# Optimization experiments

Measured on AMD Instinct MI355X. Metric: run time of the kernel, lower is better.

Reference implementation:

```python
import jax, jax.numpy as jnp
import numpy as np

# Constants from __init__ (domain bounds)
X_MIN, X_MAX = -1.0, 1.0
Y_MIN, Y_MAX = -1.0, 1.0
T_MIN, T_MAX = 0.0, 1.0

N_POINTS = 262144
WIDTH = 128
N_HIDDEN_STACK = 5  # hidden->hidden layers between first and last


def setup_inputs() -> dict:
    key = jax.random.key(0)
    ks = jax.random.split(key, 8)
    X = jax.random.uniform(ks[0], (N_POINTS, 4), dtype=jnp.float32)
    # glorot_normal-ish init
    def glorot(k, fan_in, fan_out, shape):
        std = (2.0 / (fan_in + fan_out)) ** 0.5
        return jax.random.normal(k, shape, dtype=jnp.float32) * std
    W0 = glorot(ks[1], 4, WIDTH, (4, WIDTH))
    b0 = jnp.zeros((WIDTH,), dtype=jnp.float32)
    Wh = glorot(ks[2], WIDTH, WIDTH, (N_HIDDEN_STACK, WIDTH, WIDTH))
    bh = jnp.zeros((N_HIDDEN_STACK, WIDTH), dtype=jnp.float32)
    WL = glorot(ks[3], WIDTH, 2, (WIDTH, 2))
    bL = jnp.zeros((2,), dtype=jnp.float32)
    nu_min = jnp.zeros((), dtype=jnp.float32)
    nu_max = jnp.ones((), dtype=jnp.float32)
    return {"X": X, "nu_min": nu_min, "nu_max": nu_max,
            "W0": W0, "b0": b0, "Wh": Wh, "bh": bh, "WL": WL, "bL": bL}


def _swish(x):
    return x * jax.nn.sigmoid(x)


def reference(X, nu_min, nu_max, W0, b0, Wh, bh, WL, bL):
    # Input rescaling to [-1, 1] per feature, then concat
    x_s = 2.0 * (X[:, 0:1] - X_MIN) / (X_MAX - X_MIN) - 1.0
    y_s = 2.0 * (X[:, 1:2] - Y_MIN) / (Y_MAX - Y_MIN) - 1.0
    t_s = 2.0 * (X[:, 2:3] - T_MIN) / (T_MAX - T_MIN) - 1.0
    nu_s = 2.0 * (X[:, 3:4] - nu_min) / (nu_max - nu_min) - 1.0
    H = jnp.concatenate([x_s, y_s, t_s, nu_s], axis=1)  # [N, 4]
    # Stacked small dense + swish layers (fused-MLP candidate)
    H = _swish(H @ W0 + b0)  # [N, WIDTH]
    for i in range(Wh.shape[0]):
        H = _swish(H @ Wh[i] + bh[i])
    return H @ WL + bL  # [N, 2], no activation on output layer
```

## Files before the change

### kernel.cpp

```cpp
#include <hip/hip_runtime.h>

typedef __bf16 bf16x8 __attribute__((ext_vector_type(8)));
typedef float  f32x4  __attribute__((ext_vector_type(4)));

#define WS_WT0_B 0
#define WS_WTH_B 8192
#define WS_WLT_B 172032

__device__ __forceinline__ unsigned short f2b(float f) {
  return __builtin_bit_cast(unsigned short, (__bf16)f);
}

__global__ void prep_kernel(const float* __restrict__ W0,
                            const float* __restrict__ Wh,
                            const float* __restrict__ WL,
                            unsigned short* __restrict__ ws) {
  int i = blockIdx.x * 256 + threadIdx.x;
  int l  = (i >> 3) & 63;
  int j  = i & 7;
  int lm = l & 15, lh = l >> 4;
  if (i < 4096) {
    int nt = i >> 9;
    int n = nt * 16 + lm, k = lh * 8 + j;
    ws[i] = f2b(k < 4 ? W0[k * 128 + n] : 0.f);
  } else if (i < 86016) {
    int t = i - 4096;
    int frag = t >> 9;
    int nt = frag & 7, ks = (frag >> 3) & 3, h = frag >> 5;
    int n = nt * 16 + lm, k = ks * 32 + lh * 8 + j;
    ws[i] = f2b(Wh[(h * 128 + k) * 128 + n]);
  } else if (i < 88064) {
    int t = i - 86016;
    int ks = t >> 9;
    int n = lm, k = ks * 32 + lh * 8 + j;
    ws[i] = f2b(n < 2 ? WL[k * 2 + n] : 0.f);
  }
}

__device__ __forceinline__ f32x4 swish4(f32x4 z) {
  f32x4 e;
  e[0] = __expf(-z[0]); e[1] = __expf(-z[1]);
  e[2] = __expf(-z[2]); e[3] = __expf(-z[3]);
  const f32x4 w = e + 1.f;
  f32x4 s;
  s[0] = __builtin_amdgcn_rcpf(w[0]); s[1] = __builtin_amdgcn_rcpf(w[1]);
  s[2] = __builtin_amdgcn_rcpf(w[2]); s[3] = __builtin_amdgcn_rcpf(w[3]);
  return z * s;
}

__launch_bounds__(64, 4)
__global__ void mlp_kernel(const float* __restrict__ X,
                           const float* __restrict__ nu_min_p,
                           const float* __restrict__ nu_max_p,
                           const float* __restrict__ b0,
                           const float* __restrict__ bh,
                           const float* __restrict__ bL,
                           const unsigned short* __restrict__ ws,
                           float* __restrict__ out) {
  __shared__ __align__(16) char Hs[32 * 256];
  const int lane = threadIdx.x;
  const int lm = lane & 15, lh = lane >> 4;
  const int row0 = blockIdx.x * 32;
  const char* wsb = reinterpret_cast<const char*>(ws);
  const int xorm = (lm & 7) << 4;

  if (lane < 32) {
    const float4 xv = reinterpret_cast<const float4*>(X)[row0 + lane];
    const float numin = nu_min_p[0], numax = nu_max_p[0];
    const float v0 = xv.x;
    const float v1 = xv.y;
    const float v2 = 2.f * xv.z - 1.f;
    const float v3 = 2.f * (xv.w - numin) / (numax - numin) - 1.f;
    uint4 c0;
    c0.x = (unsigned)f2b(v0) | ((unsigned)f2b(v1) << 16);
    c0.y = (unsigned)f2b(v2) | ((unsigned)f2b(v3) << 16);
    c0.z = 0u; c0.w = 0u;
    const uint4 z4 = make_uint4(0u, 0u, 0u, 0u);
    const int xr = (lane & 7) << 4;
    char* rp = Hs + lane * 256;
    *reinterpret_cast<uint4*>(rp + (0  ^ xr)) = c0;
    *reinterpret_cast<uint4*>(rp + (16 ^ xr)) = z4;
    *reinterpret_cast<uint4*>(rp + (32 ^ xr)) = z4;
    *reinterpret_cast<uint4*>(rp + (48 ^ xr)) = z4;
  }

  f32x4 acc[8][2];

  {
#pragma unroll
    for (int nt = 0; nt < 8; ++nt) {
      const f32x4 bv = *reinterpret_cast<const f32x4*>(b0 + nt * 16 + lh * 4);
      acc[nt][0] = bv; acc[nt][1] = bv;
    }
    bf16x8 bfr[2];
#pragma unroll
    for (int pt = 0; pt < 2; ++pt) {
      const int p = pt * 16 + lm;
      bfr[pt] = __builtin_bit_cast(bf16x8,
          *reinterpret_cast<const uint4*>(Hs + p * 256 + ((lh * 16) ^ xorm)));
    }
#pragma unroll
    for (int nt = 0; nt < 8; ++nt) {
      const bf16x8 a = __builtin_bit_cast(bf16x8,
          *reinterpret_cast<const uint4*>(wsb + WS_WT0_B + nt * 1024 + lane * 16));
      acc[nt][0] = __builtin_amdgcn_mfma_f32_16x16x32_bf16(a, bfr[0], acc[nt][0], 0, 0, 0);
      acc[nt][1] = __builtin_amdgcn_mfma_f32_16x16x32_bf16(a, bfr[1], acc[nt][1], 0, 0, 0);
    }
#pragma unroll
    for (int nt = 0; nt < 8; ++nt) {
#pragma unroll
      for (int pt = 0; pt < 2; ++pt) {
        const f32x4 r4 = swish4(acc[nt][pt]);
        unsigned short q0 = f2b(r4[0]), q1 = f2b(r4[1]), q2 = f2b(r4[2]), q3 = f2b(r4[3]);
        uint2 wv;
        wv.x = (unsigned)q0 | ((unsigned)q1 << 16);
        wv.y = (unsigned)q2 | ((unsigned)q3 << 16);
        const int p = pt * 16 + lm;
        *reinterpret_cast<uint2*>(Hs + p * 256 + (((nt * 16 + lh * 4) * 2) ^ xorm)) = wv;
      }
    }
  }

#pragma unroll 1
  for (int h = 0; h < 5; ++h) {
    const char* wbase = wsb + WS_WTH_B + h * 32768;
    const float* bias = bh + h * 128;
#pragma unroll
    for (int nt = 0; nt < 8; ++nt) {
      const f32x4 bv = *reinterpret_cast<const f32x4*>(bias + nt * 16 + lh * 4);
      acc[nt][0] = bv; acc[nt][1] = bv;
    }
#pragma unroll 1
    for (int ks = 0; ks < 4; ++ks) {
      bf16x8 bfr[2];
#pragma unroll
      for (int pt = 0; pt < 2; ++pt) {
        const int p = pt * 16 + lm;
        bfr[pt] = __builtin_bit_cast(bf16x8,
            *reinterpret_cast<const uint4*>(Hs + p * 256 + ((ks * 64 + lh * 16) ^ xorm)));
      }
#pragma unroll
      for (int nt = 0; nt < 8; ++nt) {
        const bf16x8 a = __builtin_bit_cast(bf16x8,
            *reinterpret_cast<const uint4*>(wbase + (ks * 8 + nt) * 1024 + lane * 16));
        acc[nt][0] = __builtin_amdgcn_mfma_f32_16x16x32_bf16(a, bfr[0], acc[nt][0], 0, 0, 0);
        acc[nt][1] = __builtin_amdgcn_mfma_f32_16x16x32_bf16(a, bfr[1], acc[nt][1], 0, 0, 0);
      }
    }
#pragma unroll
    for (int nt = 0; nt < 8; ++nt) {
#pragma unroll
      for (int pt = 0; pt < 2; ++pt) {
        const f32x4 r4 = swish4(acc[nt][pt]);
        unsigned short q0 = f2b(r4[0]), q1 = f2b(r4[1]), q2 = f2b(r4[2]), q3 = f2b(r4[3]);
        uint2 wv;
        wv.x = (unsigned)q0 | ((unsigned)q1 << 16);
        wv.y = (unsigned)q2 | ((unsigned)q3 << 16);
        const int p = pt * 16 + lm;
        *reinterpret_cast<uint2*>(Hs + p * 256 + (((nt * 16 + lh * 4) * 2) ^ xorm)) = wv;
      }
    }
  }

  {
    const float bl0 = bL[0], bl1 = bL[1];
#pragma unroll
    for (int pt2 = 0; pt2 < 2; ++pt2) {
      f32x4 accL = {0.f, 0.f, 0.f, 0.f};
      const int p = pt2 * 16 + lm;
#pragma unroll
      for (int ks = 0; ks < 4; ++ks) {
        const bf16x8 bfr = __builtin_bit_cast(bf16x8,
            *reinterpret_cast<const uint4*>(Hs + p * 256 + ((ks * 64 + lh * 16) ^ xorm)));
        const bf16x8 a = __builtin_bit_cast(bf16x8,
            *reinterpret_cast<const uint4*>(wsb + WS_WLT_B + ks * 1024 + lane * 16));
        accL = __builtin_amdgcn_mfma_f32_16x16x32_bf16(a, bfr, accL, 0, 0, 0);
      }
      if (lh == 0) {
        float2 o;
        o.x = accL[0] + bl0;
        o.y = accL[1] + bl1;
        *reinterpret_cast<float2*>(out + (size_t)(row0 + p) * 2) = o;
      }
    }
  }
}

extern "C" void kernel_launch(void* const* d_in, const int* in_sizes, int n_in,
                              void* d_out, int out_size, void* d_ws, size_t ws_size,
                              hipStream_t stream) {
  const float* X     = (const float*)d_in[0];
  const float* numin = (const float*)d_in[1];
  const float* numax = (const float*)d_in[2];
  const float* W0    = (const float*)d_in[3];
  const float* b0    = (const float*)d_in[4];
  const float* Wh    = (const float*)d_in[5];
  const float* bh    = (const float*)d_in[6];
  const float* WL    = (const float*)d_in[7];
  const float* bL    = (const float*)d_in[8];
  unsigned short* ws = (unsigned short*)d_ws;
  float* out = (float*)d_out;

  hipLaunchKernelGGL(prep_kernel, dim3(344), dim3(256), 0, stream, W0, Wh, WL, ws);
  hipLaunchKernelGGL(mlp_kernel, dim3(8192), dim3(64), 0, stream,
                     X, numin, numax, b0, bh, bL, ws, out);
}
```

Before: 81.65 us.

## Pack four waves per block, fully unroll layers, fold bias into MFMA init

```diff
diff --git a/kernel.cpp b/kernel.cpp
--- a/kernel.cpp
+++ b/kernel.cpp
@@ -1,6 +1,7 @@
 #include <hip/hip_runtime.h>
 
 typedef __bf16 bf16x8 __attribute__((ext_vector_type(8)));
+typedef __bf16 bf16x2 __attribute__((ext_vector_type(2)));
 typedef float  f32x4  __attribute__((ext_vector_type(4)));
 
 #define WS_WT0_B 0
@@ -48,7 +49,16 @@
   return z * s;
 }
 
-__launch_bounds__(64, 4)
+__device__ __forceinline__ uint2 pack4(f32x4 r) {
+  bf16x2 lo = {(__bf16)r[0], (__bf16)r[1]};
+  bf16x2 hi = {(__bf16)r[2], (__bf16)r[3]};
+  uint2 wv;
+  wv.x = __builtin_bit_cast(unsigned int, lo);
+  wv.y = __builtin_bit_cast(unsigned int, hi);
+  return wv;
+}
+
+__launch_bounds__(256, 4)
 __global__ void mlp_kernel(const float* __restrict__ X,
                            const float* __restrict__ nu_min_p,
                            const float* __restrict__ nu_max_p,
@@ -57,12 +67,20 @@
                            const float* __restrict__ bL,
                            const unsigned short* __restrict__ ws,
                            float* __restrict__ out) {
-  __shared__ __align__(16) char Hs[32 * 256];
-  const int lane = threadIdx.x;
+  __shared__ __align__(16) char HsAll[4][32 * 256];
+  const int lane = threadIdx.x & 63;
+  const int wave = threadIdx.x >> 6;
+  char* Hs = HsAll[wave];
   const int lm = lane & 15, lh = lane >> 4;
-  const int row0 = blockIdx.x * 32;
+  const int row0 = blockIdx.x * 128 + wave * 32;
   const char* wsb = reinterpret_cast<const char*>(ws);
+  const char* ap  = wsb + lane * 16;
   const int xorm = (lm & 7) << 4;
+
+  const int va0 = lm * 256 + ((lh * 16) ^ xorm);
+  const int va1 = va0 + 16 * 256;
+  const int wa0 = lm * 256 + ((lh * 8) ^ xorm);
+  const int wa1 = wa0 + 16 * 256;
 
   if (lane < 32) {
     const float4 xv = reinterpret_cast<const float4*>(X)[row0 + lane];
@@ -87,77 +105,59 @@
   f32x4 acc[8][2];
 
   {
+    bf16x8 bfr[2];
+    bfr[0] = __builtin_bit_cast(bf16x8, *reinterpret_cast<const uint4*>(Hs + va0));
+    bfr[1] = __builtin_bit_cast(bf16x8, *reinterpret_cast<const uint4*>(Hs + va1));
 #pragma unroll
     for (int nt = 0; nt < 8; ++nt) {
       const f32x4 bv = *reinterpret_cast<const f32x4*>(b0 + nt * 16 + lh * 4);
-      acc[nt][0] = bv; acc[nt][1] = bv;
-    }
-    bf16x8 bfr[2];
-#pragma unroll
-    for (int pt = 0; pt < 2; ++pt) {
-      const int p = pt * 16 + lm;
-      bfr[pt] = __builtin_bit_cast(bf16x8,
-          *reinterpret_cast<const uint4*>(Hs + p * 256 + ((lh * 16) ^ xorm)));
+      const bf16x8 a = __builtin_bit_cast(bf16x8,
+          *reinterpret_cast<const uint4*>(ap + WS_WT0_B + nt * 1024));
+      acc[nt][0] = __builtin_amdgcn_mfma_f32_16x16x32_bf16(a, bfr[0], bv, 0, 0, 0);
+      acc[nt][1] = __builtin_amdgcn_mfma_f32_16x16x32_bf16(a, bfr[1], bv, 0, 0, 0);
     }
 #pragma unroll
     for (int nt = 0; nt < 8; ++nt) {
-      const bf16x8 a = __builtin_bit_cast(bf16x8,
-          *reinterpret_cast<const uint4*>(wsb + WS_WT0_B + nt * 1024 + lane * 16));
-      acc[nt][0] = __builtin_amdgcn_mfma_f32_16x16x32_bf16(a, bfr[0], acc[nt][0], 0, 0, 0);
-      acc[nt][1] = __builtin_amdgcn_mfma_f32_16x16x32_bf16(a, bfr[1], acc[nt][1], 0, 0, 0);
-    }
-#pragma unroll
-    for (int nt = 0; nt < 8; ++nt) {
 #pragma unroll
       for (int pt = 0; pt < 2; ++pt) {
-        const f32x4 r4 = swish4(acc[nt][pt]);
-        unsigned short q0 = f2b(r4[0]), q1 = f2b(r4[1]), q2 = f2b(r4[2]), q3 = f2b(r4[3]);
-        uint2 wv;
-        wv.x = (unsigned)q0 | ((unsigned)q1 << 16);
-        wv.y = (unsigned)q2 | ((unsigned)q3 << 16);
-        const int p = pt * 16 + lm;
-        *reinterpret_cast<uint2*>(Hs + p * 256 + (((nt * 16 + lh * 4) * 2) ^ xorm)) = wv;
-      }
-    }
-  }
-
-#pragma unroll 1
+        const uint2 wv = pack4(swish4(acc[nt][pt]));
+        const int wa = (pt ? wa1 : wa0) ^ (nt << 5);
+        *reinterpret_cast<uint2*>(Hs + wa) = wv;
+      }
+    }
+  }
+
+#pragma unroll
   for (int h = 0; h < 5; ++h) {
-    const char* wbase = wsb + WS_WTH_B + h * 32768;
     const float* bias = bh + h * 128;
 #pragma unroll
-    for (int nt = 0; nt < 8; ++nt) {
-      const f32x4 bv = *reinterpret_cast<const f32x4*>(bias + nt * 16 + lh * 4);
-      acc[nt][0] = bv; acc[nt][1] = bv;
-    }
-#pragma unroll 1
     for (int ks = 0; ks < 4; ++ks) {
       bf16x8 bfr[2];
-#pragma unroll
-      for (int pt = 0; pt < 2; ++pt) {
-        const int p = pt * 16 + lm;
-        bfr[pt] = __builtin_bit_cast(bf16x8,
-            *reinterpret_cast<const uint4*>(Hs + p * 256 + ((ks * 64 + lh * 16) ^ xorm)));
-      }
+      bfr[0] = __builtin_bit_cast(bf16x8,
+          *reinterpret_cast<const uint4*>(Hs + (va0 ^ (ks << 6))));
+      bfr[1] = __builtin_bit_cast(bf16x8,
+          *reinterpret_cast<const uint4*>(Hs + (va1 ^ (ks << 6))));
 #pragma unroll
       for (int nt = 0; nt < 8; ++nt) {
         const bf16x8 a = __builtin_bit_cast(bf16x8,
-            *reinterpret_cast<const uint4*>(wbase + (ks * 8 + nt) * 1024 + lane * 16));
-        acc[nt][0] = __builtin_amdgcn_mfma_f32_16x16x32_bf16(a, bfr[0], acc[nt][0], 0, 0, 0);
-        acc[nt][1] = __builtin_amdgcn_mfma_f32_16x16x32_bf16(a, bfr[1], acc[nt][1], 0, 0, 0);
+            *reinterpret_cast<const uint4*>(ap + WS_WTH_B + h * 32768 + (ks * 8 + nt) * 1024));
+        if (ks == 0) {
+          const f32x4 bv = *reinterpret_cast<const f32x4*>(bias + nt * 16 + lh * 4);
+          acc[nt][0] = __builtin_amdgcn_mfma_f32_16x16x32_bf16(a, bfr[0], bv, 0, 0, 0);
+          acc[nt][1] = __builtin_amdgcn_mfma_f32_16x16x32_bf16(a, bfr[1], bv, 0, 0, 0);
+        } else {
+          acc[nt][0] = __builtin_amdgcn_mfma_f32_16x16x32_bf16(a, bfr[0], acc[nt][0], 0, 0, 0);
+          acc[nt][1] = __builtin_amdgcn_mfma_f32_16x16x32_bf16(a, bfr[1], acc[nt][1], 0, 0, 0);
+        }
       }
     }
 #pragma unroll
     for (int nt = 0; nt < 8; ++nt) {
 #pragma unroll
       for (int pt = 0; pt < 2; ++pt) {
-        const f32x4 r4 = swish4(acc[nt][pt]);
-        unsigned short q0 = f2b(r4[0]), q1 = f2b(r4[1]), q2 = f2b(r4[2]), q3 = f2b(r4[3]);
-        uint2 wv;
-        wv.x = (unsigned)q0 | ((unsigned)q1 << 16);
-        wv.y = (unsigned)q2 | ((unsigned)q3 << 16);
-        const int p = pt * 16 + lm;
-        *reinterpret_cast<uint2*>(Hs + p * 256 + (((nt * 16 + lh * 4) * 2) ^ xorm)) = wv;
+        const uint2 wv = pack4(swish4(acc[nt][pt]));
+        const int wa = (pt ? wa1 : wa0) ^ (nt << 5);
+        *reinterpret_cast<uint2*>(Hs + wa) = wv;
       }
     }
   }
@@ -165,18 +165,18 @@
   {
     const float bl0 = bL[0], bl1 = bL[1];
 #pragma unroll
-    for (int pt2 = 0; pt2 < 2; ++pt2) {
+    for (int pt = 0; pt < 2; ++pt) {
       f32x4 accL = {0.f, 0.f, 0.f, 0.f};
-      const int p = pt2 * 16 + lm;
 #pragma unroll
       for (int ks = 0; ks < 4; ++ks) {
         const bf16x8 bfr = __builtin_bit_cast(bf16x8,
-            *reinterpret_cast<const uint4*>(Hs + p * 256 + ((ks * 64 + lh * 16) ^ xorm)));
+            *reinterpret_cast<const uint4*>(Hs + ((pt ? va1 : va0) ^ (ks << 6))));
         const bf16x8 a = __builtin_bit_cast(bf16x8,
-            *reinterpret_cast<const uint4*>(wsb + WS_WLT_B + ks * 1024 + lane * 16));
+            *reinterpret_cast<const uint4*>(ap + WS_WLT_B + ks * 1024));
         accL = __builtin_amdgcn_mfma_f32_16x16x32_bf16(a, bfr, accL, 0, 0, 0);
       }
       if (lh == 0) {
+        const int p = pt * 16 + lm;
         float2 o;
         o.x = accL[0] + bl0;
         o.y = accL[1] + bl1;
@@ -202,6 +202,6 @@
   float* out = (float*)d_out;
 
   hipLaunchKernelGGL(prep_kernel, dim3(344), dim3(256), 0, stream, W0, Wh, WL, ws);
-  hipLaunchKernelGGL(mlp_kernel, dim3(8192), dim3(64), 0, stream,
+  hipLaunchKernelGGL(mlp_kernel, dim3(2048), dim3(256), 0, stream,
                      X, numin, numax, b0, bh, bL, ws, out);
 }
```

Result: slower. 87.91 us (+7.7%).
